# Performance work log

Hardware: AMD Instinct MI355X
Metric: run time of the kernel (lower is better)

The kernel has to match this reference:

```python
import jax, jax.numpy as jnp
import numpy as np

TAU = 0.5
BS, NQ, NT = 8, 8192, 512


def _lsa_rect(cost):
    """Rectangular linear sum assignment (shortest augmenting path, as in
    scipy.optimize.linear_sum_assignment). cost: (R, C) with R <= C.
    Returns col4row: for each row r, the assigned column."""
    R, C = cost.shape
    u = np.zeros(R, np.float64)
    v = np.zeros(C, np.float64)
    path = np.full(C, -1, np.int64)
    col4row = np.full(R, -1, np.int64)
    row4col = np.full(C, -1, np.int64)
    for cur_row in range(R):
        min_val = 0.0
        i = cur_row
        remaining = np.ones(C, bool)
        SR = np.zeros(R, bool)
        shortest = np.full(C, np.inf)
        sink = -1
        while sink == -1:
            SR[i] = True
            rem = np.nonzero(remaining)[0]
            r = min_val + cost[i, rem] - u[i] - v[rem]
            better = r < shortest[rem]
            upd = rem[better]
            shortest[upd] = r[better]
            path[upd] = i
            k = rem[np.argmin(shortest[rem])]
            min_val = shortest[k]
            remaining[k] = False
            if row4col[k] == -1:
                sink = k
            else:
                i = row4col[k]
        # dual updates
        u[cur_row] += min_val
        sr = np.nonzero(SR)[0]
        sr = sr[sr != cur_row]
        u[sr] += min_val - shortest[col4row[sr]]
        sc = ~remaining
        v[sc] -= min_val - shortest[sc]
        # augment along the alternating path
        j = sink
        while True:
            i = path[j]
            row4col[j] = i
            col4row[i], j = j, col4row[i]
            if i == cur_row:
                break
    return col4row


def setup_inputs() -> dict:
    key = jax.random.key(0)
    k1, k2, k3 = jax.random.split(key, 3)
    pred_logits = jax.random.normal(k1, (BS, NQ, 1), jnp.float32)
    # points live in a [0, 512)^2 image-coordinate box
    pred_points = jax.random.uniform(k2, (BS, NQ, 2), jnp.float32) * 512.0
    tgt_points = jax.random.uniform(k3, (BS, NT, 2), jnp.float32) * 512.0
    return {"pred_logits": pred_logits, "pred_points": pred_points,
            "tgt_points": tgt_points}


def reference(pred_logits, pred_points, tgt_points):
    # out_prob: [bs, N];  cost_class = 1 - sigmoid(logit)
    prob = jax.nn.sigmoid(pred_logits)[..., 0]
    # pairwise L2 distances [bs, N, M] (torch.cdist p=2)
    diff = pred_points[:, :, None, :] - tgt_points[:, None, :, :]
    dists = jnp.sqrt(jnp.sum(diff * diff, axis=-1))
    C = TAU * dists + (1.0 - prob)[:, :, None]
    # Hungarian assignment per sample (host-side, same math as scipy).
    Cn = np.asarray(jax.device_get(C), dtype=np.float64)
    rows, cols = [], []
    for b in range(Cn.shape[0]):
        # N > M: solve on the transpose (M rows, N cols), like scipy does.
        assigned = _lsa_rect(Cn[b].T)  # per target -> query index
        order = np.argsort(assigned)   # scipy returns row_ind sorted
        rows.append(assigned[order])
        cols.append(order)
    row_ind = jnp.asarray(np.stack(rows), jnp.int64)
    col_ind = jnp.asarray(np.stack(cols), jnp.int64)
    return C, row_ind, col_ind
```

## Files before the change

### kernel.cpp

```cpp
#include <hip/hip_runtime.h>
#include <math.h>

#define BS 8
#define NQ 8192
#define NT 512
#define NTHR 512
#define CHUNKS 16
#define NW (NTHR / 64)
#define NG 16
#define MAXL (NT + 2)
#define QCAP 4608
#define KMASK 0xFFFFFFFFFFFFE000ull
#define CFB 240

#define DINF (__builtin_inf())

typedef float vf4 __attribute__((ext_vector_type(4)));

__device__ __forceinline__ float cost_f32(float qx, float qy, float cl, float tx, float ty) {
    float dx = __fsub_rn(qx, tx);
    float dy = __fsub_rn(qy, ty);
    float d2 = __fadd_rn(__fmul_rn(dx, dx), __fmul_rn(dy, dy));
    float d  = __fsqrt_rn(d2);
    return __fadd_rn(__fmul_rn(0.5f, d), cl);
}

__device__ __forceinline__ float cls_f32(float x) {
    float s;
    if (x >= 0.0f) { float e = expf(-x); s = 1.0f / (1.0f + e); }
    else           { float e = expf(x);  s = e / (1.0f + e); }
    return __fsub_rn(1.0f, s);
}

__device__ __forceinline__ unsigned long long pack_key(double v, int idx) {
    double c = fmax(v, 0.0);
    return (((unsigned long long)__double_as_longlong(c)) & KMASK)
         | (unsigned long long)((unsigned)idx & 0x1FFFu);
}
__device__ __forceinline__ double key_val(unsigned long long k) {
    return __longlong_as_double((long long)(k & KMASK));
}

__device__ __forceinline__ void merge2(
    float a0, float a1, int ai0, int ai1, float am,
    float b0, float b1, int bi0, int bi1, float bm,
    float& o0, float& o1, int& oi0, int& oi1, float& om) {
    float s3;
    const bool bWins = (b0 < a0) || (b0 == a0 && bi0 < ai0);
    if (!bWins) {
        o0 = a0; oi0 = ai0;
        const bool a1W = (a1 < b0) || (a1 == b0 && ai1 < bi0);
        if (a1W) { o1 = a1; oi1 = ai1; s3 = b0; }
        else     { o1 = b0; oi1 = bi0; s3 = fminf(a1, b1); }
    } else {
        o0 = b0; oi0 = bi0;
        const bool b1W = (b1 < a0) || (b1 == a0 && bi1 < ai0);
        if (b1W) { o1 = b1; oi1 = bi1; s3 = a0; }
        else     { o1 = a0; oi1 = ai0; s3 = fminf(b1, a1); }
    }
    om = fminf(fminf(am, bm), s3);
}

__global__ __launch_bounds__(1024) void cand_kernel(
    const float* __restrict__ logits,
    const float* __restrict__ pred_points,
    const float* __restrict__ tgt_points,
    float* __restrict__ cls_out,
    float* __restrict__ u0, int* __restrict__ jm, float* __restrict__ bnd,
    float* __restrict__ ccost, unsigned short* __restrict__ cidx) {
    extern __shared__ char sm[];
    float2* pd = (float2*)sm;
    float*  cl = (float*)(pd + NQ);

    const int tid = threadIdx.x;
    const int b   = blockIdx.x >> 5;

    const float4* p4 = (const float4*)(pred_points + (size_t)b * NQ * 2);
    for (int t = tid; t < NQ / 2; t += 1024) ((float4*)pd)[t] = p4[t];
    for (int t = tid; t < NQ; t += 1024) cl[t] = cls_f32(logits[b * NQ + t]);
    __syncthreads();
    if ((blockIdx.x & 31) == 0) {
        for (int t = tid; t < NQ; t += 1024) cls_out[b * NQ + t] = cl[t];
    }

    const int w = tid >> 6, lane = tid & 63;
    const int i = (blockIdx.x & 31) * 16 + w;
    const int g = b * NT + i;
    const float tx = tgt_points[g * 2 + 0];
    const float ty = tgt_points[g * 2 + 1];

    float A0 = DINF, A1 = DINF, Am = DINF; int Ai0 = 0, Ai1 = 0;
    float B0 = DINF, B1 = DINF, Bm = DINF; int Bi0 = 0, Bi1 = 0;
    float C0 = DINF, C1 = DINF, Cm = DINF; int Ci0 = 0, Ci1 = 0;
    float D0 = DINF, D1 = DINF, Dm = DINF; int Di0 = 0, Di1 = 0;
    for (int k = 0; k < NQ / 256; ++k) {
        const int c = k * 256 + 4 * lane;
        const float4 p01 = ((const float4*)pd)[(c >> 1) + 0];
        const float4 p23 = ((const float4*)pd)[(c >> 1) + 1];
        const float4 c4  = ((const float4*)cl)[c >> 2];
        const float v0 = cost_f32(p01.x, p01.y, c4.x, tx, ty);
        const float v1 = cost_f32(p01.z, p01.w, c4.y, tx, ty);
        const float v2 = cost_f32(p23.x, p23.y, c4.z, tx, ty);
        const float v3 = cost_f32(p23.z, p23.w, c4.w, tx, ty);
        if (v0 < A1) { Am = A1; if (v0 < A0) { A1 = A0; Ai1 = Ai0; A0 = v0; Ai0 = c; } else { A1 = v0; Ai1 = c; } }
        else Am = fminf(Am, v0);
        if (v1 < B1) { Bm = B1; if (v1 < B0) { B1 = B0; Bi1 = Bi0; B0 = v1; Bi0 = c + 1; } else { B1 = v1; Bi1 = c + 1; } }
        else Bm = fminf(Bm, v1);
        if (v2 < C1) { Cm = C1; if (v2 < C0) { C1 = C0; Ci1 = Ci0; C0 = v2; Ci0 = c + 2; } else { C1 = v2; Ci1 = c + 2; } }
        else Cm = fminf(Cm, v2);
        if (v3 < D1) { Dm = D1; if (v3 < D0) { D1 = D0; Di1 = Di0; D0 = v3; Di0 = c + 3; } else { D1 = v3; Di1 = c + 3; } }
        else Dm = fminf(Dm, v3);
    }
    float ab0, ab1, abm; int abi0, abi1;
    float cd0, cd1, cdm; int cdi0, cdi1;
    float t0v, t1v, bb0; int t0i, t1i;
    merge2(A0, A1, Ai0, Ai1, Am, B0, B1, Bi0, Bi1, Bm, ab0, ab1, abi0, abi1, abm);
    merge2(C0, C1, Ci0, Ci1, Cm, D0, D1, Di0, Di1, Dm, cd0, cd1, cdi0, cdi1, cdm);
    merge2(ab0, ab1, abi0, abi1, abm, cd0, cd1, cdi0, cdi1, cdm, t0v, t1v, t0i, t1i, bb0);

    ((float2*)(ccost + ((size_t)g << 7)))[lane] = make_float2(t0v, t1v);
    ((ushort2*)(cidx + ((size_t)g << 7)))[lane] =
        make_ushort2((unsigned short)t0i, (unsigned short)t1i);
    float bv = t0v; int bc = t0i; float bb = bb0;
    for (int off = 32; off > 0; off >>= 1) {
        float ov = __shfl_down(bv, off, 64);
        int   oc = __shfl_down(bc, off, 64);
        float ob = __shfl_down(bb, off, 64);
        if (ov < bv || (ov == bv && oc < bc)) { bv = ov; bc = oc; }
        bb = fminf(bb, ob);
    }
    if (lane == 0) { u0[g] = bv; jm[g] = bc; bnd[g] = bb; }
}

__global__ __launch_bounds__(NTHR, 1) void fused_kernel(
    const float* __restrict__ pred_points,
    const float* __restrict__ tgt_points,
    const float* __restrict__ cls,
    const float* __restrict__ u0,
    const int* __restrict__ jm,
    const float* __restrict__ bnd,
    const float* __restrict__ ccost,
    const unsigned short* __restrict__ cidx,
    float* __restrict__ C,
    float* __restrict__ out_rows,
    float* __restrict__ out_cols) {
    const int tid = threadIdx.x;

    if (blockIdx.x >= BS) {
        const int cfid = blockIdx.x - BS;
        const int ngrp = BS * NQ / 16;
        const int g32  = tid & 31;
        for (int grp = cfid; grp < ngrp; grp += CFB) {
            const int bq = (grp << 4) + (tid >> 5);
            const int b  = bq >> 13;
            const float2 q = ((const float2*)pred_points)[bq];
            const float clv = cls[bq];
            const float* tb = tgt_points + b * NT * 2;
#pragma unroll
            for (int s = 0; s < 4; ++s) {
                const int t = g32 * 4 + s * 128;
                float4 A  = *(const float4*)(tb + t * 2);
                float4 Bv = *(const float4*)(tb + t * 2 + 4);
                vf4 r;
                r.x = cost_f32(q.x, q.y, clv, A.x,  A.y);
                r.y = cost_f32(q.x, q.y, clv, A.z,  A.w);
                r.z = cost_f32(q.x, q.y, clv, Bv.x, Bv.y);
                r.w = cost_f32(q.x, q.y, clv, Bv.z, Bv.w);
                __builtin_nontemporal_store(r, (vf4*)(C + (size_t)bq * NT + t));
            }
        }
        return;
    }

    const int b = blockIdx.x;
    extern __shared__ char smem[];
    double* v_s       = (double*)smem;
    double* u_s       = v_s + NQ;
    double* l_minv    = u_s + NT;
    double* l_v       = l_minv + MAXL;
    double* a_m2      = l_v + MAXL;
    unsigned long long* p_k = (unsigned long long*)(a_m2 + NG);
    float*  tg        = (float*)(p_k + 2 * NW);
    float*  bnd_s     = tg + NT * 2;
    float*  a_c       = bnd_s + NT;
    int*    s_int     = (int*)(a_c + NG);
    int*    a_j       = s_int + 4;
    int*    wcnt      = a_j + NG;
    short*  path_s    = (short*)(wcnt + NW);
    short*  row4col_s = path_s + NQ;
    short*  col4row_s = row4col_s + NQ;
    short*  jm_s      = col4row_s + NT;
    short*  sap_s     = jm_s + NT;
    short*  l_k       = sap_s + NT;
    short*  l_r       = l_k + MAXL;
    short*  queue_s   = l_r + MAXL;

    for (int c = tid; c < NQ; c += NTHR) row4col_s[c] = -1;
    for (int r = tid; r < NT; r += NTHR) {
        col4row_s[r] = -1;
        u_s[r]   = (double)u0[b * NT + r];
        jm_s[r]  = (short)jm[b * NT + r];
        bnd_s[r] = bnd[b * NT + r];
    }
    for (int t = tid; t < NT * 2; t += NTHR) tg[t] = tgt_points[b * NT * 2 + t];

    float  qx[CHUNKS], qy[CHUNKS], cl[CHUNKS];
    double vv[CHUNKS], sh[CHUNKS];
#pragma unroll
    for (int j = 0; j < CHUNKS; ++j) {
        int c = j * NTHR + tid;
        qx[j] = pred_points[(b * NQ + c) * 2 + 0];
        qy[j] = pred_points[(b * NQ + c) * 2 + 1];
        cl[j] = cls[b * NQ + c];
    }
    __syncthreads();

    {
        int* scratch = (int*)v_s;
        const int r = tid;
        const int jmr = jm_s[r];
        scratch[jmr] = 0x7FFFFFFF;
        __syncthreads();
        atomicMin(&scratch[jmr], r);
        __syncthreads();
        const bool conflict = (scratch[jmr] != r);
        if (!conflict) { col4row_s[r] = (short)jmr; row4col_s[jmr] = (short)r; }
        const unsigned long long bal = __ballot(conflict);
        const int lane = tid & 63, w = tid >> 6;
        if (lane == 0) wcnt[w] = __popcll(bal);
        __syncthreads();
        int pre = 0, tot = 0;
        for (int x = 0; x < NW; ++x) { if (x < w) pre += wcnt[x]; tot += wcnt[x]; }
        const int rank = pre + __popcll(bal & ((1ull << lane) - 1ull));
        if (conflict) queue_s[rank] = (short)r;
        if (tid == 0) s_int[0] = 0;
        __syncthreads();
        for (int c = tid; c < NQ; c += NTHR) v_s[c] = 0.0;
        if (tid == 0) s_int[0] = tot;
        __syncthreads();
    }

    int head = 0, tail = s_int[0], nsap = 0;
    {
        const int tail0 = tail;
        int rcap = tail0 + 48; if (rcap > 192) rcap = 192;
        const int grp = tid >> 5, gl = tid & 31;
        int rounds = 0;
        int pf_row = -1; float4 pf_cc; ushort4 pf_ci;
        while (head < tail && rounds < rcap) {
            const int nrows = (tail - head < NG) ? (tail - head) : NG;
            if (grp < nrows) {
                const int row = queue_s[head + grp];
                float4 cc; ushort4 ci;
                if (row == pf_row) { cc = pf_cc; ci = pf_ci; }
                else {
                    const int g = (b << 9) + row;
                    cc = ((const float4*)(ccost + ((size_t)g << 7)))[gl];
                    ci = ((const ushort4*)(cidx + ((size_t)g << 7)))[gl];
                }
                const unsigned long long q0 = pack_key((double)cc.x - v_s[ci.x], ci.x);
                const unsigned long long q1 = pack_key((double)cc.y - v_s[ci.y], ci.y);
                const unsigned long long q2 = pack_key((double)cc.z - v_s[ci.z], ci.z);
                const unsigned long long q3 = pack_key((double)cc.w - v_s[ci.w], ci.w);
                unsigned long long ka = q0 < q1 ? q0 : q1, kb = q0 < q1 ? q1 : q0;
                unsigned long long kc = q2 < q3 ? q2 : q3, kd = q2 < q3 ? q3 : q2;
                unsigned long long k1  = ka < kc ? ka : kc;
                unsigned long long t2_ = ka < kc ? kc : ka;
                unsigned long long t3_ = kb < kd ? kb : kd;
                unsigned long long m2b = (t2_ < t3_ ? t2_ : t3_) & KMASK;
                for (int m = 16; m > 0; m >>= 1) {
                    unsigned long long ok1 = __shfl_xor(k1, m, 32);
                    unsigned long long om2 = __shfl_xor(m2b, m, 32);
                    unsigned long long lo  = (ok1 < k1) ? ok1 : k1;
                    unsigned long long hiv = ((ok1 < k1) ? k1 : ok1) & KMASK;
                    k1 = lo;
                    if (om2 < m2b) m2b = om2;
                    if (hiv < m2b) m2b = hiv;
                }
                const double m2d = key_val(m2b);
                if (q0 == k1) a_c[grp] = cc.x;
                if (q1 == k1) a_c[grp] = cc.y;
                if (q2 == k1) a_c[grp] = cc.z;
                if (q3 == k1) a_c[grp] = cc.w;
                if (gl == 0) {
                    a_m2[grp] = m2d;
                    a_j[grp]  = (m2d < (double)bnd_s[row]) ? (int)(k1 & 0x1FFFull) : -1;
                }
            }
            {
                const int np = head + nrows + grp;
                if (np < tail) {
                    const int prow = queue_s[np];
                    const int pg = (b << 9) + prow;
                    pf_cc = ((const float4*)(ccost + ((size_t)pg << 7)))[gl];
                    pf_ci = ((const ushort4*)(cidx + ((size_t)pg << 7)))[gl];
                    pf_row = prow;
                } else pf_row = -1;
            }
            __syncthreads();
            int   cjv[NG], kov[NG], rowv[NG], act[NG];
            double m2v[NG]; float cwv[NG];
#pragma unroll
            for (int e = 0; e < NG; ++e) {
                cjv[e] = -1; act[e] = 0;
                if (e < nrows) {
                    rowv[e] = queue_s[head + e];
                    const int j1 = a_j[e];
                    if (j1 < 0) { act[e] = 3; }
                    else {
                        int dup = 0;
#pragma unroll
                        for (int x = 0; x < NG; ++x)
                            if (x < e) dup |= (cjv[x] == j1) ? 1 : 0;
                        if (dup) { act[e] = 2; }
                        else {
                            act[e] = 1; cjv[e] = j1;
                            kov[e] = row4col_s[j1];
                            m2v[e] = a_m2[e]; cwv[e] = a_c[e];
                        }
                    }
                }
            }
            __syncthreads();
            {
                int t2 = tail, ns = nsap;
#pragma unroll
                for (int e = 0; e < NG; ++e) {
                    if (act[e] == 1) {
                        const int j1 = cjv[e];
                        row4col_s[j1]     = (short)rowv[e];
                        col4row_s[rowv[e]] = (short)j1;
                        u_s[rowv[e]] = m2v[e];
                        const double nv = (double)cwv[e] - m2v[e];
                        if (nv < v_s[j1]) v_s[j1] = nv;
                        if (kov[e] >= 0) {
                            col4row_s[kov[e]] = -1;
                            queue_s[t2++] = (short)kov[e];
                        }
                    } else if (act[e] == 2) {
                        queue_s[t2++] = (short)rowv[e];
                    } else if (act[e] == 3) {
                        sap_s[ns++] = (short)rowv[e];
                    }
                }
                head += nrows; tail = t2; nsap = ns;
            }
            ++rounds;
        }
        for (int e = head; e < tail; ++e) sap_s[nsap++] = queue_s[e];
    }
    __syncthreads();

#pragma unroll
    for (int j = 0; j < CHUNKS; ++j) vv[j] = v_s[j * NTHR + tid];

    const int NL = nsap;
    for (int di = 0; di < NL; ++di) {
        const int cur_row = sap_s[di];
#pragma unroll
        for (int j = 0; j < CHUNKS; ++j) sh[j] = DINF;
        int    i    = cur_row;
        double minv = 0.0;
        int    len  = 0;
        int    sink = -1;

        for (;;) {
            const double w  = minv - u_s[i];
            const float  tx = tg[i * 2 + 0];
            const float  ty = tg[i * 2 + 1];

            double best = DINF;
            int bestc = NQ;
#pragma unroll
            for (int j = 0; j < CHUNKS; ++j) {
                const int c = j * NTHR + tid;
                float  cf = cost_f32(qx[j], qy[j], cl[j], tx, ty);
                double rr = (w + (double)cf) - vv[j];
                if (rr < sh[j]) { sh[j] = rr; path_s[c] = (short)i; }
                if (sh[j] < best) { best = sh[j]; bestc = c; }
            }
            unsigned long long bkey = pack_key(best, bestc);
            for (int off = 32; off > 0; off >>= 1) {
                unsigned long long ok = __shfl_down(bkey, off, 64);
                if (ok < bkey) bkey = ok;
            }
            const int par = len & 1;
            if ((tid & 63) == 0) p_k[par * NW + (tid >> 6)] = bkey;
            __syncthreads();
            bkey = p_k[par * NW + (tid & (NW - 1))];
            for (int m = NW >> 1; m > 0; m >>= 1) {
                unsigned long long ok = __shfl_xor(bkey, m, 64);
                if (ok < bkey) bkey = ok;
            }
            minv = key_val(bkey);
            const int k  = (int)(bkey & 0x1FFFull);
            const int rk = row4col_s[k];
            if ((k & (NTHR - 1)) == tid) {
                const int jj = k >> 9;
#pragma unroll
                for (int j = 0; j < CHUNKS; ++j)
                    if (j == jj) { l_v[len] = vv[j]; vv[j] = -DINF; sh[j] = DINF; }
            }
            if (tid == 0) { l_k[len] = (short)k; l_minv[len] = minv; l_r[len] = (short)rk; }
            ++len;
            if (rk < 0) { sink = k; break; }
            i = rk;
        }
        __syncthreads();

        const int L = len;
        for (int e = tid; e < L; e += NTHR) {
            const int rk2 = l_r[e];
            if (rk2 >= 0) u_s[rk2] += minv - l_minv[e];
        }
        if (tid == 0) u_s[cur_row] += minv;
        for (int e = 0; e < L; ++e) {
            const int k2 = l_k[e];
            if ((k2 & (NTHR - 1)) == tid) {
                const int jj = k2 >> 9;
                const double nv = l_v[e] - (minv - l_minv[e]);
#pragma unroll
                for (int j = 0; j < CHUNKS; ++j)
                    if (j == jj) vv[j] = nv;
            }
        }
        if (tid == 0) {
            int j = sink;
            for (;;) {
                const int ii = path_s[j];
                row4col_s[j] = (short)ii;
                const int t = col4row_s[ii];
                col4row_s[ii] = (short)j;
                j = t;
                if (ii == cur_row) break;
            }
        }
        __syncthreads();
    }

    for (int r = tid; r < NT; r += NTHR) {
        const int q = col4row_s[r];
        int rank = 0;
        for (int r2 = 0; r2 < NT; ++r2) rank += (col4row_s[r2] < q) ? 1 : 0;
        out_rows[b * NT + rank] = (float)q;
        out_cols[b * NT + rank] = (float)r;
    }
}

extern "C" void kernel_launch(void* const* d_in, const int* in_sizes, int n_in,
                              void* d_out, int out_size, void* d_ws, size_t ws_size,
                              hipStream_t stream) {
    const float* logits = (const float*)d_in[0];
    const float* pred   = (const float*)d_in[1];
    const float* tgt    = (const float*)d_in[2];

    float* out  = (float*)d_out;
    float* C    = out;
    float* orow = out + (size_t)BS * NQ * NT;
    float* ocol = orow + (size_t)BS * NT;

    char*  ws    = (char*)d_ws;
    float* cls   = (float*)ws;
    float* u0    = (float*)(ws + 262144);
    float* bndp  = (float*)(ws + 278528);
    int*   jmn   = (int*)(ws + 294912);
    float* ccost = (float*)(ws + 311296);
    unsigned short* cidx = (unsigned short*)(ws + 311296 + 2097152);

    const size_t smem_cand  = 98304;
    const size_t smem_fused = 132608;

    cand_kernel<<<BS * 32, 1024, smem_cand, stream>>>(
        logits, pred, tgt, cls, u0, jmn, bndp, ccost, cidx);
    fused_kernel<<<BS + CFB, NTHR, smem_fused, stream>>>(
        pred, tgt, cls, u0, jmn, bndp, ccost, cidx, C, orow, ocol);
}
```

Measured before the change: 80.86 us.

## Replace serial auction queue with parallel Jacobi-style bidding sweeps

The sequential queue-based auction phase, which processed 16 unassigned rows per round with serial conflict resolution, is replaced by sweeps. Each sweep gathers all unassigned rows, lets up to 64 of them bid in parallel using 8-lane groups, and resolves conflicts per column by taking the bid with the largest price increment. Rows whose second-best value exceeds their bound are flagged and sent to the shortest-augmenting-path phase. This cuts per-round serialization and the shared queue, at the cost of repeated full-row scans each sweep and a different sweep cap that may change how many rows fall through to the slower exact phase.

```diff
diff --git a/kernel.cpp b/kernel.cpp
--- a/kernel.cpp
+++ b/kernel.cpp
@@ -7,11 +7,10 @@
 #define NTHR 512
 #define CHUNKS 16
 #define NW (NTHR / 64)
-#define NG 16
 #define MAXL (NT + 2)
-#define QCAP 4608
 #define KMASK 0xFFFFFFFFFFFFE000ull
 #define CFB 240
+#define SWCAP 96
 
 #define DINF (__builtin_inf())
 
@@ -178,22 +177,22 @@
     double* u_s       = v_s + NQ;
     double* l_minv    = u_s + NT;
     double* l_v       = l_minv + MAXL;
-    double* a_m2      = l_v + MAXL;
-    unsigned long long* p_k = (unsigned long long*)(a_m2 + NG);
+    double* gb_m2     = l_v + MAXL;
+    unsigned long long* gb_key = (unsigned long long*)(gb_m2 + 64);
+    unsigned long long* p_k = gb_key + 64;
     float*  tg        = (float*)(p_k + 2 * NW);
     float*  bnd_s     = tg + NT * 2;
-    float*  a_c       = bnd_s + NT;
-    int*    s_int     = (int*)(a_c + NG);
-    int*    a_j       = s_int + 4;
-    int*    wcnt      = a_j + NG;
+    float*  gb_c      = bnd_s + NT;
+    int*    gb_j      = (int*)(gb_c + 64);
+    int*    wcnt      = gb_j + 64;
     short*  path_s    = (short*)(wcnt + NW);
     short*  row4col_s = path_s + NQ;
     short*  col4row_s = row4col_s + NQ;
     short*  jm_s      = col4row_s + NT;
     short*  sap_s     = jm_s + NT;
-    short*  l_k       = sap_s + NT;
+    short*  act_s     = sap_s + NT;
+    short*  l_k       = act_s + NT;
     short*  l_r       = l_k + MAXL;
-    short*  queue_s   = l_r + MAXL;
 
     for (int c = tid; c < NQ; c += NTHR) row4col_s[c] = -1;
     for (int r = tid; r < NT; r += NTHR) {
@@ -223,133 +222,129 @@
         __syncthreads();
         atomicMin(&scratch[jmr], r);
         __syncthreads();
-        const bool conflict = (scratch[jmr] != r);
-        if (!conflict) { col4row_s[r] = (short)jmr; row4col_s[jmr] = (short)r; }
-        const unsigned long long bal = __ballot(conflict);
-        const int lane = tid & 63, w = tid >> 6;
-        if (lane == 0) wcnt[w] = __popcll(bal);
-        __syncthreads();
-        int pre = 0, tot = 0;
-        for (int x = 0; x < NW; ++x) { if (x < w) pre += wcnt[x]; tot += wcnt[x]; }
-        const int rank = pre + __popcll(bal & ((1ull << lane) - 1ull));
-        if (conflict) queue_s[rank] = (short)r;
-        if (tid == 0) s_int[0] = 0;
+        if (scratch[jmr] == r) { col4row_s[r] = (short)jmr; row4col_s[jmr] = (short)r; }
         __syncthreads();
         for (int c = tid; c < NQ; c += NTHR) v_s[c] = 0.0;
-        if (tid == 0) s_int[0] = tot;
-        __syncthreads();
-    }
-
-    int head = 0, tail = s_int[0], nsap = 0;
+        __syncthreads();
+    }
+
     {
-        const int tail0 = tail;
-        int rcap = tail0 + 48; if (rcap > 192) rcap = 192;
-        const int grp = tid >> 5, gl = tid & 31;
-        int rounds = 0;
-        int pf_row = -1; float4 pf_cc; ushort4 pf_ci;
-        while (head < tail && rounds < rcap) {
-            const int nrows = (tail - head < NG) ? (tail - head) : NG;
-            if (grp < nrows) {
-                const int row = queue_s[head + grp];
-                float4 cc; ushort4 ci;
-                if (row == pf_row) { cc = pf_cc; ci = pf_ci; }
-                else {
-                    const int g = (b << 9) + row;
-                    cc = ((const float4*)(ccost + ((size_t)g << 7)))[gl];
-                    ci = ((const ushort4*)(cidx + ((size_t)g << 7)))[gl];
+        const int grp = tid >> 3, gl = tid & 7;
+        int sweeps = 0;
+        for (;;) {
+            const int r = tid;
+            const bool act = (col4row_s[r] == (short)-1);
+            const unsigned long long bal = __ballot(act);
+            if ((tid & 63) == 0) wcnt[tid >> 6] = __popcll(bal);
+            __syncthreads();
+            int pre = 0, nact = 0;
+            for (int x = 0; x < NW; ++x) {
+                if (x < (tid >> 6)) pre += wcnt[x];
+                nact += wcnt[x];
+            }
+            if (nact == 0 || sweeps >= SWCAP) break;
+            const int rank = pre + __popcll(bal & ((1ull << (tid & 63)) - 1ull));
+            if (act) act_s[rank] = (short)r;
+            __syncthreads();
+
+            const int ngr = (nact < 64) ? nact : 64;
+            if (grp < ngr) {
+                const int row = act_s[grp];
+                const int g = (b << 9) + row;
+                const float4*  cbase = (const float4*)(ccost + ((size_t)g << 7));
+                const ushort4* ibase = (const ushort4*)(cidx + ((size_t)g << 7));
+                float4 cf[4]; ushort4 ciq[4];
+#pragma unroll
+                for (int x = 0; x < 4; ++x) { cf[x] = cbase[gl * 4 + x]; ciq[x] = ibase[gl * 4 + x]; }
+                unsigned long long k1 = ~0ull, k2m = ~0ull;
+#pragma unroll
+                for (int x = 0; x < 4; ++x) {
+                    const float vc[4] = {cf[x].x, cf[x].y, cf[x].z, cf[x].w};
+                    const unsigned short ic[4] = {ciq[x].x, ciq[x].y, ciq[x].z, ciq[x].w};
+#pragma unroll
+                    for (int y = 0; y < 4; ++y) {
+                        const unsigned long long q = pack_key((double)vc[y] - v_s[ic[y]], ic[y]);
+                        if (q < k1) { k2m = k1 & KMASK; k1 = q; }
+                        else { const unsigned long long qm = q & KMASK; if (qm < k2m) k2m = qm; }
+                    }
                 }
-                const unsigned long long q0 = pack_key((double)cc.x - v_s[ci.x], ci.x);
-                const unsigned long long q1 = pack_key((double)cc.y - v_s[ci.y], ci.y);
-                const unsigned long long q2 = pack_key((double)cc.z - v_s[ci.z], ci.z);
-                const unsigned long long q3 = pack_key((double)cc.w - v_s[ci.w], ci.w);
-                unsigned long long ka = q0 < q1 ? q0 : q1, kb = q0 < q1 ? q1 : q0;
-                unsigned long long kc = q2 < q3 ? q2 : q3, kd = q2 < q3 ? q3 : q2;
-                unsigned long long k1  = ka < kc ? ka : kc;
-                unsigned long long t2_ = ka < kc ? kc : ka;
-                unsigned long long t3_ = kb < kd ? kb : kd;
-                unsigned long long m2b = (t2_ < t3_ ? t2_ : t3_) & KMASK;
-                for (int m = 16; m > 0; m >>= 1) {
-                    unsigned long long ok1 = __shfl_xor(k1, m, 32);
-                    unsigned long long om2 = __shfl_xor(m2b, m, 32);
+                for (int m = 4; m > 0; m >>= 1) {
+                    unsigned long long ok1 = __shfl_xor(k1, m, 8);
+                    unsigned long long om2 = __shfl_xor(k2m, m, 8);
                     unsigned long long lo  = (ok1 < k1) ? ok1 : k1;
                     unsigned long long hiv = ((ok1 < k1) ? k1 : ok1) & KMASK;
                     k1 = lo;
-                    if (om2 < m2b) m2b = om2;
-                    if (hiv < m2b) m2b = hiv;
+                    if (om2 < k2m) k2m = om2;
+                    if (hiv < k2m) k2m = hiv;
                 }
-                const double m2d = key_val(m2b);
-                if (q0 == k1) a_c[grp] = cc.x;
-                if (q1 == k1) a_c[grp] = cc.y;
-                if (q2 == k1) a_c[grp] = cc.z;
-                if (q3 == k1) a_c[grp] = cc.w;
-                if (gl == 0) {
-                    a_m2[grp] = m2d;
-                    a_j[grp]  = (m2d < (double)bnd_s[row]) ? (int)(k1 & 0x1FFFull) : -1;
+                const int    j1  = (int)(k1 & 0x1FFFull);
+                const double m2d = key_val(k2m);
+                if (m2d < (double)bnd_s[row]) {
+                    float csel = 0.0f;
+#pragma unroll
+                    for (int x = 0; x < 4; ++x) {
+                        if (ciq[x].x == (unsigned short)j1) csel = cf[x].x;
+                        if (ciq[x].y == (unsigned short)j1) csel = cf[x].y;
+                        if (ciq[x].z == (unsigned short)j1) csel = cf[x].z;
+                        if (ciq[x].w == (unsigned short)j1) csel = cf[x].w;
+                    }
+                    for (int m = 4; m > 0; m >>= 1) csel = fmaxf(csel, __shfl_xor(csel, m, 8));
+                    if (gl == 0) {
+                        gb_key[grp] = pack_key(m2d - (double)csel, row);
+                        gb_j[grp]   = j1;
+                        gb_m2[grp]  = m2d;
+                        gb_c[grp]   = csel;
+                    }
+                } else {
+                    if (gl == 0) { gb_j[grp] = -1; col4row_s[row] = -2; }
                 }
             }
-            {
-                const int np = head + nrows + grp;
-                if (np < tail) {
-                    const int prow = queue_s[np];
-                    const int pg = (b << 9) + prow;
-                    pf_cc = ((const float4*)(ccost + ((size_t)pg << 7)))[gl];
-                    pf_ci = ((const ushort4*)(cidx + ((size_t)pg << 7)))[gl];
-                    pf_row = prow;
-                } else pf_row = -1;
-            }
             __syncthreads();
-            int   cjv[NG], kov[NG], rowv[NG], act[NG];
-            double m2v[NG]; float cwv[NG];
-#pragma unroll
-            for (int e = 0; e < NG; ++e) {
-                cjv[e] = -1; act[e] = 0;
-                if (e < nrows) {
-                    rowv[e] = queue_s[head + e];
-                    const int j1 = a_j[e];
-                    if (j1 < 0) { act[e] = 3; }
-                    else {
-                        int dup = 0;
-#pragma unroll
-                        for (int x = 0; x < NG; ++x)
-                            if (x < e) dup |= (cjv[x] == j1) ? 1 : 0;
-                        if (dup) { act[e] = 2; }
-                        else {
-                            act[e] = 1; cjv[e] = j1;
-                            kov[e] = row4col_s[j1];
-                            m2v[e] = a_m2[e]; cwv[e] = a_c[e];
-                        }
+
+            if (grp < ngr && gb_j[grp] >= 0) {
+                const int row = act_s[grp];
+                const int j1  = gb_j[grp];
+                unsigned long long kb = gb_key[grp];
+                int win = grp;
+                for (int x = 0; x < ngr; ++x) {
+                    if (gb_j[x] == j1) {
+                        const unsigned long long kx = gb_key[x];
+                        if (kx > kb) { kb = kx; win = x; }
                     }
                 }
+                if (win == grp && gl == 0) {
+                    const int rk = row4col_s[j1];
+                    row4col_s[j1]  = (short)row;
+                    col4row_s[row] = (short)j1;
+                    u_s[row] = gb_m2[grp];
+                    const double nv = (double)gb_c[grp] - gb_m2[grp];
+                    if (nv < v_s[j1]) v_s[j1] = nv;
+                    if (rk >= 0) col4row_s[rk] = -1;
+                }
             }
             __syncthreads();
-            {
-                int t2 = tail, ns = nsap;
-#pragma unroll
-                for (int e = 0; e < NG; ++e) {
-                    if (act[e] == 1) {
-                        const int j1 = cjv[e];
-                        row4col_s[j1]     = (short)rowv[e];
-                        col4row_s[rowv[e]] = (short)j1;
-                        u_s[rowv[e]] = m2v[e];
-                        const double nv = (double)cwv[e] - m2v[e];
-                        if (nv < v_s[j1]) v_s[j1] = nv;
-                        if (kov[e] >= 0) {
-                            col4row_s[kov[e]] = -1;
-                            queue_s[t2++] = (short)kov[e];
-                        }
-                    } else if (act[e] == 2) {
-                        queue_s[t2++] = (short)rowv[e];
-                    } else if (act[e] == 3) {
-                        sap_s[ns++] = (short)rowv[e];
-                    }
-                }
-                head += nrows; tail = t2; nsap = ns;
-            }
-            ++rounds;
-        }
-        for (int e = head; e < tail; ++e) sap_s[nsap++] = queue_s[e];
+            ++sweeps;
+        }
     }
     __syncthreads();
+
+    int nsap;
+    {
+        const int r = tid;
+        const bool un = (col4row_s[r] < 0);
+        const unsigned long long bal = __ballot(un);
+        if ((tid & 63) == 0) wcnt[tid >> 6] = __popcll(bal);
+        __syncthreads();
+        int pre = 0, tot = 0;
+        for (int x = 0; x < NW; ++x) {
+            if (x < (tid >> 6)) pre += wcnt[x];
+            tot += wcnt[x];
+        }
+        const int rank = pre + __popcll(bal & ((1ull << (tid & 63)) - 1ull));
+        if (un) { sap_s[rank] = (short)r; col4row_s[r] = -1; }
+        nsap = tot;
+        __syncthreads();
+    }
 
 #pragma unroll
     for (int j = 0; j < CHUNKS; ++j) vv[j] = v_s[j * NTHR + tid];
@@ -468,7 +463,7 @@
     unsigned short* cidx = (unsigned short*)(ws + 311296 + 2097152);
 
     const size_t smem_cand  = 98304;
-    const size_t smem_fused = 132608;
+    const size_t smem_fused = 126976;
 
     cand_kernel<<<BS * 32, 1024, smem_cand, stream>>>(
         logits, pred, tgt, cls, u0, jmn, bndp, ccost, cidx);
```

Result: faster. 72.99 us (-9.7%).
